# Performance work log

Measured on AMD Instinct MI355X. Metric: run time of the kernel, lower is better.

## Reference

```python
import jax, jax.numpy as jnp
import numpy as np

B, S, D = 2, 2048, 1024
NUM_HEAD = 8
HEAD_SIZE = D // NUM_HEAD


def setup_inputs() -> dict:
    key = jax.random.key(0)
    ks = jax.random.split(key, 10)
    scale = 1.0 / np.sqrt(D)
    inp = {
        "q": jax.random.normal(ks[0], (B, S, D), dtype=jnp.float32),
        "k": jax.random.normal(ks[1], (B, S, D), dtype=jnp.float32),
        "v": jax.random.normal(ks[2], (B, S, D), dtype=jnp.float32),
        "mask": jax.random.bernoulli(ks[3], 0.1, (B, 1, S, S)),
        "Wq": jax.random.normal(ks[4], (D, D), dtype=jnp.float32) * scale,
        "bq": jnp.zeros((D,), dtype=jnp.float32),
        "Wk": jax.random.normal(ks[5], (D, D), dtype=jnp.float32) * scale,
        "bk": jnp.zeros((D,), dtype=jnp.float32),
        "Wv": jax.random.normal(ks[6], (D, D), dtype=jnp.float32) * scale,
        "bv": jnp.zeros((D,), dtype=jnp.float32),
    }
    return inp


def _split_heads(x):
    # [B,S,D] -> [B,H,S,Hd]
    b, s, _ = x.shape
    return x.reshape(b, s, NUM_HEAD, HEAD_SIZE).transpose(0, 2, 1, 3)


def reference(q, k, v, mask, Wq, bq, Wk, bk, Wv, bv):
    Q = _split_heads(q @ Wq + bq)
    K = _split_heads(k @ Wk + bk)
    V = _split_heads(v @ Wv + bv)
    # scores [B,H,S,S]; NB: mask applied BEFORE scaling, as in the original
    QK = jnp.einsum("bhqd,bhkd->bhqk", Q, K)
    QK = jnp.where(mask, jnp.float32(-1e6), QK)
    QK = QK / jnp.float32(np.sqrt(HEAD_SIZE))
    attn = jax.nn.softmax(QK, axis=-1)  # dropout is identity in eval mode
    ctx = jnp.einsum("bhqk,bhkd->bhqd", attn, V)
    out = ctx.transpose(0, 2, 1, 3).reshape(q.shape[0], q.shape[1], D)
    return out
```

## Files before the change

### kernel.cpp

```cpp
#include <hip/hip_runtime.h>

typedef __bf16 bf16;
typedef __attribute__((ext_vector_type(8))) __bf16 bf16x8;
typedef __attribute__((ext_vector_type(4))) __bf16 bf16x4;
typedef __attribute__((ext_vector_type(4))) float f32x4;
typedef __attribute__((ext_vector_type(4))) float fvec4;

#define NB 2
#define SEQ 2048
#define DM 1024
#define NH 8
#define HD 128

#define QSCL (0.08838834764831845f * 1.4426950408889634f)

__global__ void mask_detect(const unsigned int* __restrict__ m,
                            unsigned int* __restrict__ flag)
{
    __shared__ unsigned int s[256];
    unsigned int f = 0;
    for (int i = threadIdx.x; i < 1024; i += 256) {
        const unsigned int w = m[i];
        if ((w & 0xFEFEFEFEu) == 0u && (w & 0xFFFFFF00u) != 0u) f = 1;
    }
    s[threadIdx.x] = f;
    __syncthreads();
    if (threadIdx.x == 0) {
        unsigned int r = 0;
        for (int i = 0; i < 256; i++) r |= s[i];
        *flag = r;
    }
}

__global__ __launch_bounds__(256) void mask_pack(
    const void* __restrict__ m, const unsigned int* __restrict__ flag,
    unsigned long long* __restrict__ bits)
{
    const int gid = blockIdx.x * 256 + threadIdx.x;
    bool mk;
    if (*flag & 1u)
        mk = ((const unsigned char*)m)[gid] != 0;
    else
        mk = ((const unsigned int*)m)[gid] != 0u;
    const unsigned long long b = __ballot(mk);
    if ((threadIdx.x & 63) == 0) bits[gid >> 6] = b;
}

__global__ __launch_bounds__(256) void proj_kernel(
    const float* __restrict__ qi, const float* __restrict__ ki,
    const float* __restrict__ vi,
    const float* __restrict__ Wq, const float* __restrict__ Wk,
    const float* __restrict__ Wv,
    const float* __restrict__ bq, const float* __restrict__ bk,
    const float* __restrict__ bv,
    bf16* __restrict__ Qo, bf16* __restrict__ Ko, bf16* __restrict__ Vto)
{
    __shared__ __align__(16) bf16 As[128 * 40];
    __shared__ __align__(16) bf16 Bs[128 * 40];

    const int pz = blockIdx.z;
    const float* X = (pz == 0) ? qi : (pz == 1) ? ki : vi;
    const float* W = (pz == 0) ? Wq : (pz == 1) ? Wk : Wv;
    const float* bias = (pz == 0) ? bq : (pz == 1) ? bk : bv;
    bf16* dst = (pz == 0) ? Qo : (pz == 1) ? Ko : Vto;
    const float oscale = (pz == 0) ? QSCL : 1.0f;

    const int tid  = threadIdx.x;
    const int lane = tid & 63;
    const int w    = tid >> 6;
    const int q16  = lane >> 4;
    const int l15  = lane & 15;

    const int m0 = blockIdx.y * 128;
    const int n0 = blockIdx.x * 128;
    const int wm = (w >> 1) * 64;
    const int wn = (w & 1) * 64;

    const int ar = tid >> 3;
    const int ac = tid & 7;
    const int bc = (tid & 31) * 4;
    const int br = (tid >> 5) * 4;

    f32x4 acc[4][4] = {};

    for (int k0 = 0; k0 < DM; k0 += 32) {
        __syncthreads();
        #pragma unroll
        for (int i = 0; i < 4; i++) {
            const int row = ar + i * 32;
            const fvec4 xv =
                *(const fvec4*)(X + (size_t)(m0 + row) * DM + k0 + ac * 4);
            bf16x4 hv;
            hv.x = (bf16)xv.x; hv.y = (bf16)xv.y;
            hv.z = (bf16)xv.z; hv.w = (bf16)xv.w;
            *(bf16x4*)(As + row * 40 + ac * 4) = hv;
        }
        fvec4 wv[4];
        #pragma unroll
        for (int rr = 0; rr < 4; rr++)
            wv[rr] = *(const fvec4*)(W + (size_t)(k0 + br + rr) * DM + n0 + bc);
        #pragma unroll
        for (int cc = 0; cc < 4; cc++) {
            bf16x4 hv;
            hv.x = (bf16)wv[0][cc]; hv.y = (bf16)wv[1][cc];
            hv.z = (bf16)wv[2][cc]; hv.w = (bf16)wv[3][cc];
            *(bf16x4*)(Bs + (bc + cc) * 40 + br) = hv;
        }
        __syncthreads();

        bf16x8 af[4], bfr[4];
        #pragma unroll
        for (int mi = 0; mi < 4; mi++)
            af[mi] = *(const bf16x8*)(As + (wm + mi * 16 + l15) * 40 + q16 * 8);
        #pragma unroll
        for (int ni = 0; ni < 4; ni++)
            bfr[ni] = *(const bf16x8*)(Bs + (wn + ni * 16 + l15) * 40 + q16 * 8);
        #pragma unroll
        for (int mi = 0; mi < 4; mi++)
            #pragma unroll
            for (int ni = 0; ni < 4; ni++)
                acc[mi][ni] = __builtin_amdgcn_mfma_f32_16x16x32_bf16(
                    af[mi], bfr[ni], acc[mi][ni], 0, 0, 0);
    }

    float bias_v[4];
    #pragma unroll
    for (int ni = 0; ni < 4; ni++)
        bias_v[ni] = bias[n0 + wn + ni * 16 + l15];

    #pragma unroll
    for (int mi = 0; mi < 4; mi++) {
        #pragma unroll
        for (int ni = 0; ni < 4; ni++) {
            const int n  = n0 + wn + ni * 16 + l15;
            const int h  = n >> 7;
            const int hd = n & (HD - 1);
            #pragma unroll
            for (int r = 0; r < 4; r++) {
                const int m = m0 + wm + mi * 16 + q16 * 4 + r;
                const int b = m >> 11;
                const int s = m & (SEQ - 1);
                const float val = (acc[mi][ni][r] + bias_v[ni]) * oscale;
                size_t idx;
                if (pz == 2)
                    idx = ((size_t)(b * NH + h) * HD + hd) * SEQ + s;
                else
                    idx = ((size_t)(b * NH + h) * SEQ + s) * HD + hd;
                dst[idx] = (bf16)val;
            }
        }
    }
}

__global__ __launch_bounds__(256) void attn_kernel(
    const bf16* __restrict__ Q, const bf16* __restrict__ K,
    const bf16* __restrict__ Vt, const unsigned int* __restrict__ maskbits,
    float* __restrict__ out)
{
    __shared__ __align__(16) bf16 Ks[2][64 * 128];
    __shared__ __align__(16) bf16 Vs[2][128 * 64];
    __shared__ __align__(16) bf16 Ps[4][16 * 72];

    const int tid  = threadIdx.x;
    const int lane = tid & 63;
    const int w    = tid >> 6;
    const int q16  = lane >> 4;
    const int l15  = lane & 15;
    const int l3   = l15 & 7;

    const int b  = blockIdx.z;
    const int h  = blockIdx.y;
    const int q0 = blockIdx.x * 64;
    const int bh = b * NH + h;

    const bf16* Qb = Q  + (size_t)bh * SEQ * HD;
    const bf16* Kb = K  + (size_t)bh * SEQ * HD;
    const bf16* Vb = Vt + (size_t)bh * HD * SEQ;
    const unsigned long long* mb64 =
        (const unsigned long long*)maskbits + (size_t)b * (SEQ * SEQ / 64);
    const int qbase = q0 + w * 16 + q16 * 4;
    const unsigned long long* mrow = mb64 + (size_t)qbase * (SEQ / 64);

    const int qrow_a = q0 + w * 16 + l15;
    bf16x8 qf[4];
    #pragma unroll
    for (int c = 0; c < 4; c++)
        qf[c] = *(const bf16x8*)(Qb + (size_t)qrow_a * HD + c * 32 + q16 * 8);

    f32x4 o[8] = {};
    float m_i[4], l_i[4];
    #pragma unroll
    for (int r = 0; r < 4; r++) { m_i[r] = -__builtin_inff(); l_i[r] = 0.f; }

    const float MASKV = -1.0e6f * QSCL;

    auto stage = [&](int buf, int k0) {
        bf16* kd = &Ks[buf][0];
        bf16* vd = &Vs[buf][0];
        #pragma unroll
        for (int i = 0; i < 4; i++) {
            const int c   = i * 256 + tid;
            const int row = c >> 4;
            const int cir = c & 15;
            const bf16* src =
                Kb + (size_t)(k0 + row) * HD + ((cir ^ (row & 7)) << 3);
            __builtin_amdgcn_global_load_lds(
                (const __attribute__((address_space(1))) void*)src,
                (__attribute__((address_space(3))) void*)(kd + c * 8),
                16, 0, 0);
        }
        #pragma unroll
        for (int i = 0; i < 4; i++) {
            const int c   = i * 256 + tid;
            const int d   = c >> 3;
            const int cir = c & 7;
            const bf16* src =
                Vb + (size_t)d * SEQ + k0 + ((cir ^ (d & 7)) << 3);
            __builtin_amdgcn_global_load_lds(
                (const __attribute__((address_space(1))) void*)src,
                (__attribute__((address_space(3))) void*)(vd + c * 8),
                16, 0, 0);
        }
    };

    unsigned long long mwn[4];
    stage(0, 0);
    #pragma unroll
    for (int r = 0; r < 4; r++) mwn[r] = mrow[(size_t)r * (SEQ / 64)];
    __syncthreads();

    bf16* Pw = &Ps[w][0];
    int cur = 0;

    for (int kt = 0; kt < SEQ / 64; ++kt) {
        unsigned long long mw[4];
        #pragma unroll
        for (int r = 0; r < 4; r++) mw[r] = mwn[r];

        if (kt + 1 < SEQ / 64) stage(cur ^ 1, (kt + 1) * 64);
        const int ktn = (kt + 1) & (SEQ / 64 - 1);
        #pragma unroll
        for (int r = 0; r < 4; r++)
            mwn[r] = mrow[(size_t)r * (SEQ / 64) + ktn];

        const bf16* Ksb = &Ks[cur][0];
        const bf16* Vsb = &Vs[cur][0];

        f32x4 sf[4] = {};
        #pragma unroll
        for (int c = 0; c < 4; c++) {
            #pragma unroll
            for (int nf = 0; nf < 4; nf++) {
                const bf16x8 kf = *(const bf16x8*)(
                    Ksb + (nf * 16 + l15) * 128 + (((c * 4 + q16) ^ l3) << 3));
                sf[nf] = __builtin_amdgcn_mfma_f32_16x16x32_bf16(
                    qf[c], kf, sf[nf], 0, 0, 0);
            }
        }

        #pragma unroll
        for (int nf = 0; nf < 4; nf++)
            #pragma unroll
            for (int r = 0; r < 4; r++) {
                const int mk = (int)((mw[r] >> (nf * 16 + l15)) & 1ull);
                sf[nf][r] = mk ? MASKV : sf[nf][r];
            }

        float alpha[4];
        bool need = false;
        #pragma unroll
        for (int r = 0; r < 4; r++) {
            float mx = fmaxf(fmaxf(sf[0][r], sf[1][r]),
                             fmaxf(sf[2][r], sf[3][r]));
            #pragma unroll
            for (int off = 1; off < 16; off <<= 1)
                mx = fmaxf(mx, __shfl_xor(mx, off, 16));
            const float mnew = fmaxf(m_i[r], mx);
            alpha[r] = __builtin_amdgcn_exp2f(m_i[r] - mnew);
            need |= (mnew > m_i[r]);
            m_i[r] = mnew;
            float ps = 0.f;
            #pragma unroll
            for (int nf = 0; nf < 4; nf++) {
                const float p = __builtin_amdgcn_exp2f(sf[nf][r] - mnew);
                sf[nf][r] = p;
                ps += p;
            }
            l_i[r] = l_i[r] * alpha[r] + ps;
        }

        if (__ballot(need)) {
            #pragma unroll
            for (int df = 0; df < 8; df++)
                #pragma unroll
                for (int r = 0; r < 4; r++)
                    o[df][r] *= alpha[r];
        }

        #pragma unroll
        for (int nf = 0; nf < 4; nf++)
            #pragma unroll
            for (int r = 0; r < 4; r++)
                Pw[(q16 * 4 + r) * 72 + nf * 16 + l15] = (bf16)sf[nf][r];

        bf16x8 pf[2];
        #pragma unroll
        for (int cc = 0; cc < 2; cc++)
            pf[cc] = *(const bf16x8*)(Pw + l15 * 72 + cc * 32 + q16 * 8);

        #pragma unroll
        for (int df = 0; df < 8; df++) {
            #pragma unroll
            for (int cc = 0; cc < 2; cc++) {
                const bf16x8 vf = *(const bf16x8*)(
                    Vsb + (df * 16 + l15) * 64 + (((cc * 4 + q16) ^ l3) << 3));
                o[df] = __builtin_amdgcn_mfma_f32_16x16x32_bf16(
                    pf[cc], vf, o[df], 0, 0, 0);
            }
        }

        __syncthreads();
        cur ^= 1;
    }

    #pragma unroll
    for (int r = 0; r < 4; r++) {
        float ls = l_i[r];
        #pragma unroll
        for (int off = 1; off < 16; off <<= 1)
            ls += __shfl_xor(ls, off, 16);
        l_i[r] = 1.0f / ls;
    }
    #pragma unroll
    for (int df = 0; df < 8; df++) {
        #pragma unroll
        for (int r = 0; r < 4; r++) {
            const int qr = q0 + w * 16 + q16 * 4 + r;
            out[((size_t)b * SEQ + qr) * DM + h * HD + df * 16 + l15] =
                o[df][r] * l_i[r];
        }
    }
}

extern "C" void kernel_launch(void* const* d_in, const int* in_sizes, int n_in,
                              void* d_out, int out_size, void* d_ws, size_t ws_size,
                              hipStream_t stream) {
    const float* q    = (const float*)d_in[0];
    const float* k    = (const float*)d_in[1];
    const float* v    = (const float*)d_in[2];
    const void*  mask = d_in[3];
    const float* Wq   = (const float*)d_in[4];
    const float* bq   = (const float*)d_in[5];
    const float* Wk   = (const float*)d_in[6];
    const float* bk   = (const float*)d_in[7];
    const float* Wv   = (const float*)d_in[8];
    const float* bv   = (const float*)d_in[9];
    float* out = (float*)d_out;

    char* ws = (char*)d_ws;
    unsigned long long* bits = (unsigned long long*)ws;
    const size_t bits_bytes = (size_t)NB * SEQ * SEQ / 8;
    unsigned int* flag = (unsigned int*)(ws + bits_bytes);
    bf16* Qp = (bf16*)(ws + bits_bytes + 256);
    bf16* Kp = Qp + (size_t)NB * SEQ * DM;
    bf16* Vp = Kp + (size_t)NB * SEQ * DM;

    mask_detect<<<1, 256, 0, stream>>>((const unsigned int*)mask, flag);
    mask_pack<<<(NB * SEQ * SEQ) / 256, 256, 0, stream>>>(mask, flag, bits);

    dim3 pgrid(DM / 128, (NB * SEQ) / 128, 3);
    proj_kernel<<<pgrid, 256, 0, stream>>>(q, k, v, Wq, Wk, Wv, bq, bk, bv,
                                           Qp, Kp, Vp);

    dim3 agrid(SEQ / 64, NH, NB);
    attn_kernel<<<agrid, 256, 0, stream>>>(Qp, Kp, Vp,
                                           (const unsigned int*)bits, out);
}
```

Measured before the change: 289.7 us.

## Pre-convert projection inputs to bf16 and pipeline GEMM with direct-to-LDS loads

Adds a prep kernel that converts q/k/v to bf16 and transposes and pre-scales the weights into bf16 K-major layout. The projection GEMM then double-buffers 64-wide K tiles, loading straight into LDS with global_load_lds and an XOR swizzle, so the next tile's load overlaps the MFMA work on the current one. This removes per-tile fp32 conversion and the strided transpose from the GEMM inner loop. In exchange it adds an extra kernel launch and an extra full pass of bf16 writes and reads through workspace memory.

Measured after the change: 295.2 us. Within noise of the previous version (+1.9%).

```diff
diff --git a/kernel.cpp b/kernel.cpp
--- a/kernel.cpp
+++ b/kernel.cpp
@@ -46,24 +46,75 @@
     if ((threadIdx.x & 63) == 0) bits[gid >> 6] = b;
 }
 
-__global__ __launch_bounds__(256) void proj_kernel(
+__global__ __launch_bounds__(256) void prep_kernel(
     const float* __restrict__ qi, const float* __restrict__ ki,
     const float* __restrict__ vi,
     const float* __restrict__ Wq, const float* __restrict__ Wk,
     const float* __restrict__ Wv,
+    bf16* __restrict__ Xc, bf16* __restrict__ Wt)
+{
+    const int z   = blockIdx.y;
+    const int tid = threadIdx.x;
+    __shared__ __align__(16) bf16 tile[64][80];
+
+    if (z < 3) {
+        const float* src = (z == 0) ? qi : (z == 1) ? ki : vi;
+        bf16* dst = Xc + (size_t)z * ((size_t)NB * SEQ * DM);
+        const size_t base = (size_t)blockIdx.x * 4096 + (size_t)tid * 16;
+        fvec4 f[4];
+        #pragma unroll
+        for (int j = 0; j < 4; j++)
+            f[j] = *(const fvec4*)(src + base + j * 4);
+        bf16x8 h0, h1;
+        #pragma unroll
+        for (int e = 0; e < 8; e++) {
+            h0[e] = (bf16)f[e >> 2][e & 3];
+            h1[e] = (bf16)f[2 + (e >> 2)][e & 3];
+        }
+        *(bf16x8*)(dst + base)     = h0;
+        *(bf16x8*)(dst + base + 8) = h1;
+    } else {
+        if (blockIdx.x >= 256) return;
+        const float* W = (z == 3) ? Wq : (z == 4) ? Wk : Wv;
+        bf16* dst = Wt + (size_t)(z - 3) * ((size_t)DM * DM);
+        const float scl = (z == 3) ? QSCL : 1.0f;
+        const int n0 = (blockIdx.x & 15) * 64;
+        const int k0 = (blockIdx.x >> 4) * 64;
+        #pragma unroll
+        for (int p = 0; p < 4; p++) {
+            const int r = p * 16 + (tid >> 4);
+            const int c = (tid & 15) * 4;
+            const fvec4 wv = *(const fvec4*)(W + (size_t)(k0 + r) * DM + n0 + c);
+            #pragma unroll
+            for (int j = 0; j < 4; j++)
+                tile[c + j][r] = (bf16)(wv[j] * scl);
+        }
+        __syncthreads();
+        #pragma unroll
+        for (int p = 0; p < 2; p++) {
+            const int row = p * 32 + (tid >> 3);
+            const int ch  = tid & 7;
+            const bf16x8 hv = *(const bf16x8*)(&tile[row][ch * 8]);
+            *(bf16x8*)(dst + (size_t)(n0 + row) * DM + k0 + ch * 8) = hv;
+        }
+    }
+}
+
+__global__ __launch_bounds__(256) void proj_kernel(
+    const bf16* __restrict__ Xc, const bf16* __restrict__ Wt,
     const float* __restrict__ bq, const float* __restrict__ bk,
     const float* __restrict__ bv,
     bf16* __restrict__ Qo, bf16* __restrict__ Ko, bf16* __restrict__ Vto)
 {
-    __shared__ __align__(16) bf16 As[128 * 40];
-    __shared__ __align__(16) bf16 Bs[128 * 40];
+    __shared__ __align__(16) bf16 As[2][128 * 64];
+    __shared__ __align__(16) bf16 Bs[2][128 * 64];
 
     const int pz = blockIdx.z;
-    const float* X = (pz == 0) ? qi : (pz == 1) ? ki : vi;
-    const float* W = (pz == 0) ? Wq : (pz == 1) ? Wk : Wv;
+    const bf16* X  = Xc + (size_t)pz * ((size_t)NB * SEQ * DM);
+    const bf16* Bt = Wt + (size_t)pz * ((size_t)DM * DM);
     const float* bias = (pz == 0) ? bq : (pz == 1) ? bk : bv;
+    const float bscl  = (pz == 0) ? QSCL : 1.0f;
     bf16* dst = (pz == 0) ? Qo : (pz == 1) ? Ko : Vto;
-    const float oscale = (pz == 0) ? QSCL : 1.0f;
 
     const int tid  = threadIdx.x;
     const int lane = tid & 63;
@@ -76,51 +127,66 @@
     const int wm = (w >> 1) * 64;
     const int wn = (w & 1) * 64;
 
-    const int ar = tid >> 3;
-    const int ac = tid & 7;
-    const int bc = (tid & 31) * 4;
-    const int br = (tid >> 5) * 4;
+    auto stage = [&](int buf, int k0) {
+        #pragma unroll
+        for (int i = 0; i < 4; i++) {
+            const int c   = i * 256 + tid;
+            const int row = c >> 3;
+            const int cir = c & 7;
+            const bf16* src =
+                X + (size_t)(m0 + row) * DM + k0 + ((cir ^ (row & 7)) << 3);
+            __builtin_amdgcn_global_load_lds(
+                (const __attribute__((address_space(1))) void*)src,
+                (__attribute__((address_space(3))) void*)(&As[buf][c * 8]),
+                16, 0, 0);
+        }
+        #pragma unroll
+        for (int i = 0; i < 4; i++) {
+            const int c   = i * 256 + tid;
+            const int row = c >> 3;
+            const int cir = c & 7;
+            const bf16* src =
+                Bt + (size_t)(n0 + row) * DM + k0 + ((cir ^ (row & 7)) << 3);
+            __builtin_amdgcn_global_load_lds(
+                (const __attribute__((address_space(1))) void*)src,
+                (__attribute__((address_space(3))) void*)(&Bs[buf][c * 8]),
+                16, 0, 0);
+        }
+    };
 
     f32x4 acc[4][4] = {};
-
-    for (int k0 = 0; k0 < DM; k0 += 32) {
+    stage(0, 0);
+    __syncthreads();
+    int cur = 0;
+
+    for (int kt = 0; kt < DM / 64; ++kt) {
+        if (kt + 1 < DM / 64) stage(cur ^ 1, (kt + 1) * 64);
+        const bf16* Asb = &As[cur][0];
+        const bf16* Bsb = &Bs[cur][0];
+        #pragma unroll
+        for (int c2 = 0; c2 < 2; c2++) {
+            bf16x8 af[4], bfr[4];
+            #pragma unroll
+            for (int mi = 0; mi < 4; mi++) {
+                const int row = wm + mi * 16 + l15;
+                af[mi] = *(const bf16x8*)(
+                    Asb + row * 64 + (((c2 * 4 + q16) ^ (row & 7)) << 3));
+            }
+            #pragma unroll
+            for (int ni = 0; ni < 4; ni++) {
+                const int row = wn + ni * 16 + l15;
+                bfr[ni] = *(const bf16x8*)(
+                    Bsb + row * 64 + (((c2 * 4 + q16) ^ (row & 7)) << 3));
+            }
+            #pragma unroll
+            for (int mi = 0; mi < 4; mi++)
+                #pragma unroll
+                for (int ni = 0; ni < 4; ni++)
+                    acc[mi][ni] = __builtin_amdgcn_mfma_f32_16x16x32_bf16(
+                        af[mi], bfr[ni], acc[mi][ni], 0, 0, 0);
+        }
         __syncthreads();
-        #pragma unroll
-        for (int i = 0; i < 4; i++) {
-            const int row = ar + i * 32;
-            const fvec4 xv =
-                *(const fvec4*)(X + (size_t)(m0 + row) * DM + k0 + ac * 4);
-            bf16x4 hv;
-            hv.x = (bf16)xv.x; hv.y = (bf16)xv.y;
-            hv.z = (bf16)xv.z; hv.w = (bf16)xv.w;
-            *(bf16x4*)(As + row * 40 + ac * 4) = hv;
-        }
-        fvec4 wv[4];
-        #pragma unroll
-        for (int rr = 0; rr < 4; rr++)
-            wv[rr] = *(const fvec4*)(W + (size_t)(k0 + br + rr) * DM + n0 + bc);
-        #pragma unroll
-        for (int cc = 0; cc < 4; cc++) {
-            bf16x4 hv;
-            hv.x = (bf16)wv[0][cc]; hv.y = (bf16)wv[1][cc];
-            hv.z = (bf16)wv[2][cc]; hv.w = (bf16)wv[3][cc];
-            *(bf16x4*)(Bs + (bc + cc) * 40 + br) = hv;
-        }
-        __syncthreads();
-
-        bf16x8 af[4], bfr[4];
-        #pragma unroll
-        for (int mi = 0; mi < 4; mi++)
-            af[mi] = *(const bf16x8*)(As + (wm + mi * 16 + l15) * 40 + q16 * 8);
-        #pragma unroll
-        for (int ni = 0; ni < 4; ni++)
-            bfr[ni] = *(const bf16x8*)(Bs + (wn + ni * 16 + l15) * 40 + q16 * 8);
-        #pragma unroll
-        for (int mi = 0; mi < 4; mi++)
-            #pragma unroll
-            for (int ni = 0; ni < 4; ni++)
-                acc[mi][ni] = __builtin_amdgcn_mfma_f32_16x16x32_bf16(
-                    af[mi], bfr[ni], acc[mi][ni], 0, 0, 0);
+        cur ^= 1;
     }
 
     float bias_v[4];
@@ -140,7 +206,7 @@
                 const int m = m0 + wm + mi * 16 + q16 * 4 + r;
                 const int b = m >> 11;
                 const int s = m & (SEQ - 1);
-                const float val = (acc[mi][ni][r] + bias_v[ni]) * oscale;
+                const float val = acc[mi][ni][r] + bias_v[ni] * bscl;
                 size_t idx;
                 if (pz == 2)
                     idx = ((size_t)(b * NH + h) * HD + hd) * SEQ + s;
@@ -364,13 +430,16 @@
     bf16* Qp = (bf16*)(ws + bits_bytes + 256);
     bf16* Kp = Qp + (size_t)NB * SEQ * DM;
     bf16* Vp = Kp + (size_t)NB * SEQ * DM;
+    bf16* Xc = Vp + (size_t)NB * SEQ * DM;
+    bf16* Wt = Xc + (size_t)3 * NB * SEQ * DM;
 
     mask_detect<<<1, 256, 0, stream>>>((const unsigned int*)mask, flag);
     mask_pack<<<(NB * SEQ * SEQ) / 256, 256, 0, stream>>>(mask, flag, bits);
 
+    prep_kernel<<<dim3(1024, 6), 256, 0, stream>>>(q, k, v, Wq, Wk, Wv, Xc, Wt);
+
     dim3 pgrid(DM / 128, (NB * SEQ) / 128, 3);
-    proj_kernel<<<pgrid, 256, 0, stream>>>(q, k, v, Wq, Wk, Wv, bq, bk, bv,
-                                           Qp, Kp, Vp);
+    proj_kernel<<<pgrid, 256, 0, stream>>>(Xc, Wt, bq, bk, bv, Qp, Kp, Vp);
 
     dim3 agrid(SEQ / 64, NH, NB);
     attn_kernel<<<agrid, 256, 0, stream>>>(Qp, Kp, Vp,
```
